# Optimization experiments

Measured on AMD Instinct MI355X. Metric: run time of the kernel, lower is better.

Reference implementation:

```python
import jax, jax.numpy as jnp
import numpy as np

D_MODEL = 1024
N_HEADS = 16
WINDOW = 256
SSM_N = 256
EPS = 1e-5


def _layernorm(x, g, b):
    m = x.mean(-1, keepdims=True)
    v = ((x - m) ** 2).mean(-1, keepdims=True)
    return (x - m) / jnp.sqrt(v + EPS) * g + b


def _sliding_window_attn(Q, K, V, W):
    # Q,K,V: [B,h,T,dh]; exact sliding-window causal attention (keys q-W+1..q)
    B, h, T, dh = Q.shape
    nb = T // W
    Qb = Q.reshape(B, h, nb, W, dh)
    pad = jnp.zeros((B, h, W, dh), Q.dtype)
    Kp = jnp.concatenate([pad, K], axis=2)  # [B,h,T+W,dh]
    Kprev = Kp[:, :, :T].reshape(B, h, nb, W, dh)
    Kcur = K.reshape(B, h, nb, W, dh)
    Kwin = jnp.concatenate([Kprev, Kcur], axis=3)  # [B,h,nb,2W,dh]
    Vp = jnp.concatenate([pad, V], axis=2)
    Vprev = Vp[:, :, :T].reshape(B, h, nb, W, dh)
    Vcur = V.reshape(B, h, nb, W, dh)
    Vwin = jnp.concatenate([Vprev, Vcur], axis=3)
    scores = jnp.einsum('bhnid,bhnjd->bhnij', Qb, Kwin) / jnp.sqrt(jnp.asarray(dh, Q.dtype))
    i = jnp.arange(W)[:, None]
    j = jnp.arange(2 * W)[None, :]
    blk = jnp.arange(nb)[:, None, None]
    # key global pos = blk*W - W + j ; valid iff i < j <= i+W and key pos >= 0
    mask = (j > i) & (j <= i + W) & (blk * W - W + j >= 0)  # [nb,W,2W]
    neg = jnp.asarray(jnp.finfo(scores.dtype).min, scores.dtype)
    scores = jnp.where(mask[None, None], scores, neg)
    p = jax.nn.softmax(scores, axis=-1)
    out = jnp.einsum('bhnij,bhnjd->bhnid', p, Vwin)
    return out.reshape(B, h, T, dh)


def _forward(x, ssm_state, ln1_g, ln1_b, ln2_g, ln2_b, wq, bq, wk, bk, wv, bv,
             wo, bo, wg, bg, A, Bw, Cw, w1, b1, w2, b2):
    B, T, d = x.shape
    h = N_HEADS
    dh = d // h
    xn = _layernorm(x, ln1_g, ln1_b)
    # windowed attention path
    Q = (xn @ wq + bq).reshape(B, T, h, dh).transpose(0, 2, 1, 3)
    K = (xn @ wk + bk).reshape(B, T, h, dh).transpose(0, 2, 1, 3)
    V = (xn @ wv + bv).reshape(B, T, h, dh).transpose(0, 2, 1, 3)
    ao = _sliding_window_attn(Q, K, V, WINDOW)
    y_attn = ao.transpose(0, 2, 1, 3).reshape(B, T, d) @ wo + bo
    # SSM path: s_t = tanh(A)*s_{t-1} + B x_t ; y_t = C s_t
    alpha = jnp.tanh(A)
    u = xn @ Bw  # [B,T,N]
    def step(s, u_t):
        s = alpha * s + u_t
        return s, s
    new_state, states = jax.lax.scan(step, ssm_state, u.transpose(1, 0, 2))
    y_ssm = states.transpose(1, 0, 2) @ Cw  # [B,T,d]
    # gated fusion + residual
    g = jax.nn.sigmoid(xn @ wg + bg)
    y = g * y_attn + (1.0 - g) * y_ssm
    x = x + y
    # Pre-LN MLP
    x2 = _layernorm(x, ln2_g, ln2_b)
    x = x + jax.nn.gelu(x2 @ w1 + b1, approximate=False) @ w2 + b2
    return x, new_state


def setup_inputs() -> dict:
    key = jax.random.key(0)
    ks = jax.random.split(key, 16)
    B, T, d, N = 2, 2048, D_MODEL, SSM_N
    s = 0.02
    inp = {
        'x': jax.random.normal(ks[0], (B, T, d), jnp.float32),
        'ssm_state': jnp.zeros((B, N), jnp.float32),
        'ln1_g': jnp.ones((d,), jnp.float32),
        'ln1_b': jnp.zeros((d,), jnp.float32),
        'ln2_g': jnp.ones((d,), jnp.float32),
        'ln2_b': jnp.zeros((d,), jnp.float32),
        'wq': jax.random.normal(ks[1], (d, d), jnp.float32) * s,
        'bq': jnp.zeros((d,), jnp.float32),
        'wk': jax.random.normal(ks[2], (d, d), jnp.float32) * s,
        'bk': jnp.zeros((d,), jnp.float32),
        'wv': jax.random.normal(ks[3], (d, d), jnp.float32) * s,
        'bv': jnp.zeros((d,), jnp.float32),
        'wo': jax.random.normal(ks[4], (d, d), jnp.float32) * s,
        'bo': jnp.zeros((d,), jnp.float32),
        'wg': jax.random.normal(ks[5], (d, d), jnp.float32) * s,
        'bg': jnp.zeros((d,), jnp.float32),
        'A': jax.random.uniform(ks[6], (N,), jnp.float32, -0.1, 0.1),
        'Bw': jax.random.normal(ks[7], (d, N), jnp.float32) * s,
        'Cw': jax.random.normal(ks[8], (N, d), jnp.float32) * s,
        'w1': jax.random.normal(ks[9], (d, 4 * d), jnp.float32) * s,
        'b1': jnp.zeros((4 * d,), jnp.float32),
        'w2': jax.random.normal(ks[10], (4 * d, d), jnp.float32) * s,
        'b2': jnp.zeros((d,), jnp.float32),
    }
    return inp


def reference(x, ssm_state, ln1_g, ln1_b, ln2_g, ln2_b, wq, bq, wk, bk, wv, bv,
              wo, bo, wg, bg, A, Bw, Cw, w1, b1, w2, b2):
    return _forward(x, ssm_state, ln1_g, ln1_b, ln2_g, ln2_b, wq, bq, wk, bk,
                    wv, bv, wo, bo, wg, bg, A, Bw, Cw, w1, b1, w2, b2)
```

## Files before the change

kernel.cpp:

```cpp
#include <hip/hip_runtime.h>
#include <math.h>

#define BB 2
#define TT 2048
#define DD 1024
#define HH 16
#define DH 64
#define WW 256
#define NN 256
#define ROWS (BB*TT)
#define ROWSZ ((size_t)ROWS*DD)
#define NQU 4352

typedef unsigned short u16;
typedef __attribute__((ext_vector_type(8))) short short8;
typedef __attribute__((ext_vector_type(4))) float f32x4;

__device__ __forceinline__ float bf2f(u16 h) {
    union { unsigned int u; float f; } c; c.u = ((unsigned int)h) << 16; return c.f;
}
__device__ __forceinline__ u16 f2bf(float f) {
    union { float f; unsigned int u; } c; c.f = f;
    unsigned int r = c.u + 0x7fffu + ((c.u >> 16) & 1u);
    return (u16)(r >> 16);
}

__device__ __forceinline__ void gld16(const void* g, void* l) {
    __builtin_amdgcn_global_load_lds(
        (const __attribute__((address_space(1))) void*)g,
        (__attribute__((address_space(3))) void*)l, 16, 0, 0);
}

#define WAITB(N) asm volatile("s_waitcnt vmcnt(" #N ")\n\ts_barrier" ::: "memory")

__global__ __launch_bounds__(256) void ln_kernel(const float* __restrict__ x,
                                                 const float* __restrict__ g,
                                                 const float* __restrict__ b,
                                                 u16* __restrict__ out) {
    int row = blockIdx.x;
    int t = threadIdx.x;
    const float4* xr = (const float4*)(x + (size_t)row * DD);
    float4 v4 = xr[t];
    float s  = v4.x + v4.y + v4.z + v4.w;
    float s2 = v4.x*v4.x + v4.y*v4.y + v4.z*v4.z + v4.w*v4.w;
    #pragma unroll
    for (int o = 32; o > 0; o >>= 1) { s += __shfl_xor(s, o); s2 += __shfl_xor(s2, o); }
    __shared__ float red[2][4];
    int wid = t >> 6, lane = t & 63;
    if (lane == 0) { red[0][wid] = s; red[1][wid] = s2; }
    __syncthreads();
    s  = red[0][0] + red[0][1] + red[0][2] + red[0][3];
    s2 = red[1][0] + red[1][1] + red[1][2] + red[1][3];
    float mean = s * (1.0f / DD);
    float var  = s2 * (1.0f / DD) - mean * mean;
    float inv  = rsqrtf(var + 1e-5f);
    const float4* g4 = (const float4*)g;
    const float4* b4 = (const float4*)b;
    float4 gg = g4[t], bb = b4[t];
    float o0 = (v4.x - mean) * inv * gg.x + bb.x;
    float o1 = (v4.y - mean) * inv * gg.y + bb.y;
    float o2 = (v4.z - mean) * inv * gg.z + bb.z;
    float o3 = (v4.w - mean) * inv * gg.w + bb.w;
    uint2 packed;
    packed.x = (unsigned)f2bf(o0) | ((unsigned)f2bf(o1) << 16);
    packed.y = (unsigned)f2bf(o2) | ((unsigned)f2bf(o3) << 16);
    *(uint2*)(out + (size_t)row * DD + 4 * t) = packed;
}

__global__ __launch_bounds__(256) void tconv_all(
    const float* __restrict__ wq, const float* __restrict__ wk,
    const float* __restrict__ wv, const float* __restrict__ wg,
    const float* __restrict__ Bw, const float* __restrict__ wo,
    const float* __restrict__ Cw, const float* __restrict__ w1,
    const float* __restrict__ w2,
    u16* __restrict__ wqkvgut, u16* __restrict__ wot, u16* __restrict__ cwt,
    u16* __restrict__ w1t, u16* __restrict__ w2t) {
    int tile = blockIdx.x;
    const float* src; u16* dst; int K, N, tx, ty;
    if (tile < 4096) {
        int seg = tile >> 10, tl = tile & 1023;
        src = (seg == 0) ? wq : (seg == 1) ? wk : (seg == 2) ? wv : wg;
        dst = wqkvgut + (size_t)seg * 1024 * 1024;
        K = 1024; N = 1024; tx = tl & 31; ty = tl >> 5;
    } else if (tile < 4352) {
        int tl = tile - 4096;
        src = Bw; dst = wqkvgut + (size_t)4096 * 1024;
        K = 1024; N = 256; tx = tl & 7; ty = tl >> 3;
    } else if (tile < 5376) {
        int tl = tile - 4352;
        src = wo; dst = wot; K = 1024; N = 1024; tx = tl & 31; ty = tl >> 5;
    } else if (tile < 5632) {
        int tl = tile - 5376;
        src = Cw; dst = cwt; K = 256; N = 1024; tx = tl & 31; ty = tl >> 5;
    } else if (tile < 9728) {
        int tl = tile - 5632;
        src = w1; dst = w1t; K = 1024; N = 4096; tx = tl & 127; ty = tl >> 7;
    } else {
        int tl = tile - 9728;
        src = w2; dst = w2t; K = 4096; N = 1024; tx = tl & 31; ty = tl >> 5;
    }
    __shared__ float ts[32][33];
    int n0 = tx * 32, k0 = ty * 32;
    int tc = threadIdx.x & 31, tr = threadIdx.x >> 5;
    #pragma unroll
    for (int i = tr; i < 32; i += 8)
        ts[i][tc] = src[(size_t)(k0 + i) * N + n0 + tc];
    __syncthreads();
    #pragma unroll
    for (int i = tr; i < 32; i += 8)
        dst[(size_t)(n0 + i) * K + k0 + tc] = f2bf(ts[tc][i]);
}

__global__ __launch_bounds__(256) void bias_init(const float* __restrict__ bq,
                                                 const float* __restrict__ bk,
                                                 const float* __restrict__ bv,
                                                 const float* __restrict__ bg,
                                                 float* __restrict__ dst) {
    int i = blockIdx.x * 256 + threadIdx.x;
    if (i >= NQU) return;
    float v = 0.f;
    if (i < 1024) v = bq[i];
    else if (i < 2048) v = bk[i - 1024];
    else if (i < 3072) v = bv[i - 2048];
    else if (i < 4096) v = bg[i - 3072];
    dst[i] = v;
}

__device__ __forceinline__ void gemm_core_pipe(const u16* __restrict__ A,
                                               const u16* __restrict__ Bt,
                                               int K, int kiters, int kofs,
                                               int m0, int n0,
                                               short (*Als)[128][32],
                                               short (*Bls)[128][32],
                                               int t, f32x4 acc[4][4]) {
    int lane = t & 63, w = t >> 6;
    int wr = w >> 1, wc = w & 1;
    int jq = lane >> 4, rq = lane & 15;
    int swzb = (jq ^ ((rq >> 1) & 3)) << 4;
    const char* gA[2]; const char* gB[2];
    int lofs[2];
    #pragma unroll
    for (int i = 0; i < 2; i++) {
        int s = i * 256 + t;
        int r = s >> 2, p = s & 3;
        int j = p ^ ((r >> 1) & 3);
        gA[i] = (const char*)(A + (size_t)(m0 + r) * K + kofs) + j * 16;
        gB[i] = (const char*)(Bt + (size_t)(n0 + r) * K + kofs) + j * 16;
        lofs[i] = s * 16;
    }
    #pragma unroll
    for (int i = 0; i < 2; i++) {
        gld16(gA[i], (char*)(Als + 0) + lofs[i]);
        gld16(gB[i], (char*)(Bls + 0) + lofs[i]);
    }
    if (kiters > 1) {
        #pragma unroll
        for (int i = 0; i < 2; i++) {
            gld16(gA[i] + 64, (char*)(Als + 1) + lofs[i]);
            gld16(gB[i] + 64, (char*)(Bls + 1) + lofs[i]);
        }
    }
    for (int kt = 0; kt < kiters; kt++) {
        if (kt + 1 < kiters) { WAITB(4); } else { WAITB(0); }
        if (kt + 2 < kiters) {
            int q = (kt + 2) % 3;
            size_t ko = (size_t)(kt + 2) * 64;
            #pragma unroll
            for (int i = 0; i < 2; i++) {
                gld16(gA[i] + ko, (char*)(Als + q) + lofs[i]);
                gld16(gB[i] + ko, (char*)(Bls + q) + lofs[i]);
            }
        }
        int p = kt % 3;
        const char* Ab = (const char*)(Als + p);
        const char* Bb = (const char*)(Bls + p);
        short8 af[4], bfr[4];
        #pragma unroll
        for (int i = 0; i < 4; i++) {
            af[i]  = *(const short8*)(Ab + (wr * 64 + i * 16 + rq) * 64 + swzb);
            bfr[i] = *(const short8*)(Bb + (wc * 64 + i * 16 + rq) * 64 + swzb);
        }
        #pragma unroll
        for (int i = 0; i < 4; i++)
            #pragma unroll
            for (int jn = 0; jn < 4; jn++)
                acc[i][jn] = __builtin_amdgcn_mfma_f32_16x16x32_bf16(af[i], bfr[jn], acc[i][jn], 0, 0, 0);
    }
}

template<int ACT, bool OUTBF, bool SPLIT>
__global__ __launch_bounds__(256) void mgemm64(const u16* __restrict__ A,
                                               const u16* __restrict__ Bt,
                                               const float* __restrict__ bias,
                                               void* __restrict__ C,
                                               int M, int N, int K, int Kslice,
                                               int mtiles, int ntiles, int PM, int PN) {
    __shared__ __align__(16) short Als[3][128][32];
    __shared__ __align__(16) short Bls[3][128][32];
    int t = threadIdx.x;
    int l = blockIdx.x;
    int xcd = l & 7, li = l >> 3;
    int rm = mtiles / PM, rn = ntiles / PN;
    int xm = xcd % PM, xn = xcd / PM;
    int mt = xm * rm + li % rm;
    int nt = xn * rn + li / rm;
    int m0 = mt * 128, n0 = nt * 128;
    int z = SPLIT ? blockIdx.y : 0;
    f32x4 acc[4][4];
    #pragma unroll
    for (int i = 0; i < 4; i++)
        #pragma unroll
        for (int j = 0; j < 4; j++)
            acc[i][j] = (f32x4){0.f, 0.f, 0.f, 0.f};
    gemm_core_pipe(A, Bt, K, Kslice >> 5, z * Kslice, m0, n0, Als, Bls, t, acc);

    int lane = t & 63, w = t >> 6;
    int wr = w >> 1, wc = w & 1;
    int jq = lane >> 4, rq = lane & 15;
    u16* Cb = OUTBF ? ((u16*)C + (SPLIT ? (size_t)z * M * N : (size_t)0)) : nullptr;
    float* Cf = (float*)C;
    #pragma unroll
    for (int i = 0; i < 4; i++) {
        int rowb = m0 + wr * 64 + i * 16 + jq * 4;
        #pragma unroll
        for (int jn = 0; jn < 4; jn++) {
            int col = n0 + wc * 64 + jn * 16 + rq;
            float bv = bias ? bias[col] : 0.f;
            #pragma unroll
            for (int rr = 0; rr < 4; rr++) {
                float v = acc[i][jn][rr] + bv;
                if (ACT == 1) v = 0.5f * v * (1.0f + erff(v * 0.70710678118654752f));
                size_t off = (size_t)(rowb + rr) * N + col;
                if (OUTBF) Cb[off] = f2bf(v);
                else Cf[off] = v;
            }
        }
    }
}

__global__ __launch_bounds__(256) void proj3(const u16* __restrict__ ao,
                                             const u16* __restrict__ states,
                                             const u16* __restrict__ wot,
                                             const u16* __restrict__ cwt,
                                             const float* __restrict__ bo,
                                             u16* __restrict__ ya0,
                                             u16* __restrict__ ya1,
                                             float* __restrict__ ys) {
    __shared__ __align__(16) short Als[3][128][32];
    __shared__ __align__(16) short Bls[3][128][32];
    int t = threadIdx.x;
    int m0 = blockIdx.y * 128, n0 = blockIdx.x * 128;
    int z = blockIdx.z;
    const u16* A; const u16* Bt; int K, kofs, kiters;
    if (z < 2) { A = ao; Bt = wot; K = 1024; kofs = z * 512; kiters = 16; }
    else       { A = states; Bt = cwt; K = 256; kofs = 0; kiters = 8; }
    f32x4 acc[4][4];
    #pragma unroll
    for (int i = 0; i < 4; i++)
        #pragma unroll
        for (int j = 0; j < 4; j++)
            acc[i][j] = (f32x4){0.f, 0.f, 0.f, 0.f};
    gemm_core_pipe(A, Bt, K, kiters, kofs, m0, n0, Als, Bls, t, acc);

    int lane = t & 63, w = t >> 6;
    int wr = w >> 1, wc = w & 1;
    int jq = lane >> 4, rq = lane & 15;
    u16* dst = (z == 0) ? ya0 : ya1;
    #pragma unroll
    for (int i = 0; i < 4; i++) {
        int rowb = m0 + wr * 64 + i * 16 + jq * 4;
        #pragma unroll
        for (int jn = 0; jn < 4; jn++) {
            int col = n0 + wc * 64 + jn * 16 + rq;
            float bv = (z == 0) ? bo[col] : 0.f;
            #pragma unroll
            for (int rr = 0; rr < 4; rr++) {
                float v = acc[i][jn][rr] + bv;
                size_t off = (size_t)(rowb + rr) * DD + col;
                if (z < 2) dst[off] = f2bf(v);
                else ys[off] = v;
            }
        }
    }
}

__global__ __launch_bounds__(256) void attn_scan(const u16* __restrict__ QKVG,
                                                 u16* __restrict__ O,
                                                 const float* __restrict__ Assm,
                                                 const float* __restrict__ s0,
                                                 u16* __restrict__ states,
                                                 float* __restrict__ s_out) {
    __shared__ __align__(16) short Qs[8][64][8];
    __shared__ __align__(16) short Ks[8][64][8];
    __shared__ __align__(16) short Vt[64][72];
    __shared__ __align__(16) short Ps[4][16][72];

    if (blockIdx.x >= 1024) {
        int idx = (blockIdx.x - 1024) * 256 + threadIdx.x;
        int n = idx & 255;
        int c = (idx >> 8) & 31;
        int b = idx >> 13;
        float alpha = tanhf(Assm[n]);
        int t0 = c * 64;
        float s = (c == 0) ? s0[b * NN + n] : 0.f;
        const u16* up = QKVG + (size_t)(b * TT) * NQU + 4096 + n;
        if (c > 0) {
            #pragma unroll
            for (int k = 8; k >= 1; k--)
                s = alpha * s + bf2f(up[(size_t)(t0 - k) * NQU]);
        }
        u16* sp = states + (size_t)(b * TT) * NN + n;
        for (int t = t0; t < t0 + 64; t++) {
            s = alpha * s + bf2f(up[(size_t)t * NQU]);
            sp[(size_t)t * NN] = f2bf(s);
        }
        if (c == 31) s_out[b * NN + n] = s;
        return;
    }

    int blk = blockIdx.x;
    int qb = blk & 31;
    int h  = (blk >> 5) & 15;
    int b  = blk >> 9;
    int q0 = qb * 64;
    int t = threadIdx.x, lane = t & 63, w = t >> 6;
    int rq = lane & 15, jq = lane >> 4;

    const size_t RS = NQU;

    #pragma unroll
    for (int i = 0; i < 2; i++) {
        int c = 2 * w + i;
        const u16* g = QKVG + (size_t)(b * TT + q0 + lane) * RS + h * 64 + c * 8;
        gld16(g, (char*)Qs + c * 1024);
    }

    f32x4 Oa[4];
    #pragma unroll
    for (int tj = 0; tj < 4; tj++) Oa[tj] = (f32x4){0.f, 0.f, 0.f, 0.f};
    float mrow[4], lrow[4];
    #pragma unroll
    for (int r = 0; r < 4; r++) { mrow[r] = -1e30f; lrow[r] = 0.f; }

    int c0 = 4 - (q0 >> 6); if (c0 < 0) c0 = 0;

    for (int ci = c0; ci < 5; ci++) {
        int kbase = q0 - 256 + ci * 64;
        #pragma unroll
        for (int i = 0; i < 2; i++) {
            int c = 2 * w + i;
            const u16* g = QKVG + (size_t)(b * TT + kbase + lane) * RS + 1024 + h * 64 + c * 8;
            gld16(g, (char*)Ks + c * 1024);
        }
        #pragma unroll
        for (int i = 0; i < 2; i++) {
            int dhg = i * 4 + w;
            uint4 v = *(const uint4*)(QKVG + (size_t)(b * TT + kbase + lane) * RS + 2048 + h * 64 + dhg * 8);
            const u16* pv = (const u16*)&v;
            #pragma unroll
            for (int j = 0; j < 8; j++) Vt[dhg * 8 + j][lane] = (short)pv[j];
        }
        __syncthreads();

        short8 qf[2];
        #pragma unroll
        for (int s = 0; s < 2; s++)
            qf[s] = *(const short8*)&Qs[4 * s + jq][w * 16 + rq][0];

        f32x4 S[4];
        #pragma unroll
        for (int tj = 0; tj < 4; tj++) S[tj] = (f32x4){0.f, 0.f, 0.f, 0.f};
        #pragma unroll
        for (int s = 0; s < 2; s++)
            #pragma unroll
            for (int tj = 0; tj < 4; tj++) {
                short8 kf = *(const short8*)&Ks[4 * s + jq][tj * 16 + rq][0];
                S[tj] = __builtin_amdgcn_mfma_f32_16x16x32_bf16(qf[s], kf, S[tj], 0, 0, 0);
            }

        #pragma unroll
        for (int r = 0; r < 4; r++) {
            int q = q0 + w * 16 + jq * 4 + r;
            float sv[4];
            #pragma unroll
            for (int tj = 0; tj < 4; tj++) {
                int kp = kbase + tj * 16 + rq;
                float x = S[tj][r] * 0.125f;
                bool valid = (kp <= q) && (kp > q - WW);
                sv[tj] = valid ? x : -1e30f;
            }
            float cm = fmaxf(fmaxf(sv[0], sv[1]), fmaxf(sv[2], sv[3]));
            #pragma unroll
            for (int o = 1; o < 16; o <<= 1) cm = fmaxf(cm, __shfl_xor(cm, o));
            float mn = fmaxf(mrow[r], cm);
            bool any = mn > -1e29f;
            float al = any ? __expf(mrow[r] - mn) : 1.f;
            float ps = 0.f;
            #pragma unroll
            for (int tj = 0; tj < 4; tj++) {
                float p = any ? __expf(sv[tj] - mn) : 0.f;
                ps += p;
                Ps[w][jq * 4 + r][tj * 16 + rq] = (short)f2bf(p);
            }
            #pragma unroll
            for (int o = 1; o < 16; o <<= 1) ps += __shfl_xor(ps, o);
            lrow[r] = lrow[r] * al + ps;
            mrow[r] = mn;
            #pragma unroll
            for (int tj = 0; tj < 4; tj++) Oa[tj][r] *= al;
        }

        #pragma unroll
        for (int s = 0; s < 2; s++) {
            short8 pf = *(const short8*)&Ps[w][rq][32 * s + 8 * jq];
            #pragma unroll
            for (int tj = 0; tj < 4; tj++) {
                short8 vf = *(const short8*)&Vt[tj * 16 + rq][32 * s + 8 * jq];
                Oa[tj] = __builtin_amdgcn_mfma_f32_16x16x32_bf16(pf, vf, Oa[tj], 0, 0, 0);
            }
        }
        __syncthreads();
    }

    #pragma unroll
    for (int r = 0; r < 4; r++) {
        int q = q0 + w * 16 + jq * 4 + r;
        float inv = 1.f / lrow[r];
        #pragma unroll
        for (int tj = 0; tj < 4; tj++)
            O[(size_t)(b * TT + q) * DD + h * 64 + tj * 16 + rq] = f2bf(Oa[tj][r] * inv);
    }
}

__global__ __launch_bounds__(256) void fuse_ln2(const float* __restrict__ x,
                                                const u16* __restrict__ QKVG,
                                                const u16* __restrict__ ya0,
                                                const u16* __restrict__ ya1,
                                                const float* __restrict__ ys,
                                                const float* __restrict__ g2,
                                                const float* __restrict__ b2,
                                                float* __restrict__ out,
                                                u16* __restrict__ x2n) {
    int row = blockIdx.x, t = threadIdx.x;
    float4 xv = ((const float4*)(x + (size_t)row * DD))[t];
    uint2 gw = *(const uint2*)(QKVG + (size_t)row * NQU + 3072 + 4 * t);
    uint2 a0 = *(const uint2*)(ya0 + (size_t)row * DD + 4 * t);
    uint2 a1 = *(const uint2*)(ya1 + (size_t)row * DD + 4 * t);
    float4 sv = ((const float4*)(ys + (size_t)row * DD))[t];
    u16 gh[4] = {(u16)(gw.x & 0xffff), (u16)(gw.x >> 16), (u16)(gw.y & 0xffff), (u16)(gw.y >> 16)};
    u16 ah[4] = {(u16)(a0.x & 0xffff), (u16)(a0.x >> 16), (u16)(a0.y & 0xffff), (u16)(a0.y >> 16)};
    u16 bh[4] = {(u16)(a1.x & 0xffff), (u16)(a1.x >> 16), (u16)(a1.y & 0xffff), (u16)(a1.y >> 16)};
    float xe[4] = {xv.x, xv.y, xv.z, xv.w};
    float se[4] = {sv.x, sv.y, sv.z, sv.w};
    float o[4];
    #pragma unroll
    for (int e = 0; e < 4; e++) {
        float g = 1.0f / (1.0f + __expf(-bf2f(gh[e])));
        float a = bf2f(ah[e]) + bf2f(bh[e]);
        o[e] = xe[e] + g * a + (1.0f - g) * se[e];
    }
    float s = o[0] + o[1] + o[2] + o[3];
    float s2 = o[0]*o[0] + o[1]*o[1] + o[2]*o[2] + o[3]*o[3];
    #pragma unroll
    for (int off = 32; off > 0; off >>= 1) { s += __shfl_xor(s, off); s2 += __shfl_xor(s2, off); }
    __shared__ float red[2][4];
    int wid = t >> 6, lane = t & 63;
    if (lane == 0) { red[0][wid] = s; red[1][wid] = s2; }
    __syncthreads();
    s  = red[0][0] + red[0][1] + red[0][2] + red[0][3];
    s2 = red[1][0] + red[1][1] + red[1][2] + red[1][3];
    float mean = s * (1.0f / DD);
    float var  = s2 * (1.0f / DD) - mean * mean;
    float inv  = rsqrtf(var + 1e-5f);
    float4 gg = ((const float4*)g2)[t];
    float4 bb = ((const float4*)b2)[t];
    float ge[4] = {gg.x, gg.y, gg.z, gg.w};
    float be[4] = {bb.x, bb.y, bb.z, bb.w};
    float4 ov = {o[0], o[1], o[2], o[3]};
    ((float4*)(out + (size_t)row * DD))[t] = ov;
    u16 nh[4];
    #pragma unroll
    for (int e = 0; e < 4; e++) nh[e] = f2bf((o[e] - mean) * inv * ge[e] + be[e]);
    uint2 packed;
    packed.x = (unsigned)nh[0] | ((unsigned)nh[1] << 16);
    packed.y = (unsigned)nh[2] | ((unsigned)nh[3] << 16);
    *(uint2*)(x2n + (size_t)row * DD + 4 * t) = packed;
}

__global__ __launch_bounds__(256) void mlp2_reduce(const u16* __restrict__ pbase,
                                                   const float* __restrict__ b2,
                                                   float* __restrict__ out) {
    size_t i4 = (size_t)blockIdx.x * 256 + threadIdx.x;
    float4 o = ((float4*)out)[i4];
    float4 bb = ((const float4*)b2)[i4 & 255];
    float acc0 = bb.x, acc1 = bb.y, acc2 = bb.z, acc3 = bb.w;
    #pragma unroll
    for (int z = 0; z < 4; z++) {
        uint2 p = ((const uint2*)(pbase + (size_t)z * ROWSZ))[i4];
        acc0 += bf2f((u16)(p.x & 0xffff));
        acc1 += bf2f((u16)(p.x >> 16));
        acc2 += bf2f((u16)(p.y & 0xffff));
        acc3 += bf2f((u16)(p.y >> 16));
    }
    o.x += acc0; o.y += acc1; o.z += acc2; o.w += acc3;
    ((float4*)out)[i4] = o;
}

extern "C" void kernel_launch(void* const* d_in, const int* in_sizes, int n_in,
                              void* d_out, int out_size, void* d_ws, size_t ws_size,
                              hipStream_t stream) {
    const float* x     = (const float*)d_in[0];
    const float* sst   = (const float*)d_in[1];
    const float* ln1g  = (const float*)d_in[2];
    const float* ln1b  = (const float*)d_in[3];
    const float* ln2g  = (const float*)d_in[4];
    const float* ln2b  = (const float*)d_in[5];
    const float* wq    = (const float*)d_in[6];
    const float* bq    = (const float*)d_in[7];
    const float* wk    = (const float*)d_in[8];
    const float* bk    = (const float*)d_in[9];
    const float* wv    = (const float*)d_in[10];
    const float* bv    = (const float*)d_in[11];
    const float* wo    = (const float*)d_in[12];
    const float* bo    = (const float*)d_in[13];
    const float* wg    = (const float*)d_in[14];
    const float* bg    = (const float*)d_in[15];
    const float* A     = (const float*)d_in[16];
    const float* Bw    = (const float*)d_in[17];
    const float* Cw    = (const float*)d_in[18];
    const float* w1    = (const float*)d_in[19];
    const float* b1    = (const float*)d_in[20];
    const float* w2    = (const float*)d_in[21];
    const float* b2    = (const float*)d_in[22];

    float* out = (float*)d_out;
    char* ws = (char*)d_ws;
    const size_t KBs = 1024;

    u16*   QKVGU  = (u16*)(ws);
    u16*   ya0b   = (u16*)(ws + 34816 * KBs);
    u16*   ya1b   = (u16*)(ws + 43008 * KBs);
    float* ys     = (float*)(ws + 51200 * KBs);
    u16*   parts  = ya0b;
    u16*   xn     = (u16*)(ws + 67584 * KBs);
    u16*   ao     = (u16*)(ws + 75776 * KBs);
    u16*   states = (u16*)(ws + 83968 * KBs);
    u16*   wqkvgut= (u16*)(ws + 86016 * KBs);
    u16*   wot    = (u16*)(ws + 94720 * KBs);
    u16*   cwt    = (u16*)(ws + 96768 * KBs);
    u16*   w1t    = (u16*)(ws + 97280 * KBs);
    u16*   w2t    = (u16*)(ws + 105472 * KBs);
    float* biasq  = (float*)(ws + 113664 * KBs);
    u16*   x2n    = xn;
    u16*   h1     = QKVGU;

    float* new_state_out = out + ROWSZ;

    hipLaunchKernelGGL(tconv_all, dim3(13824), dim3(256), 0, stream,
                       wq, wk, wv, wg, Bw, wo, Cw, w1, w2,
                       wqkvgut, wot, cwt, w1t, w2t);
    hipLaunchKernelGGL(bias_init, dim3(17), dim3(256), 0, stream, bq, bk, bv, bg, biasq);

    hipLaunchKernelGGL(ln_kernel, dim3(ROWS), dim3(256), 0, stream, x, ln1g, ln1b, xn);
    hipLaunchKernelGGL((mgemm64<0,true,false>), dim3(1088, 1), dim3(256), 0, stream,
                       xn, wqkvgut, biasq, (void*)QKVGU, ROWS, NQU, 1024, 1024,
                       32, 34, 4, 2);
    hipLaunchKernelGGL(attn_scan, dim3(1088), dim3(256), 0, stream,
                       QKVGU, ao, A, sst, states, new_state_out);
    hipLaunchKernelGGL(proj3, dim3(8, 32, 3), dim3(256), 0, stream,
                       ao, states, wot, cwt, bo, ya0b, ya1b, ys);
    hipLaunchKernelGGL(fuse_ln2, dim3(ROWS), dim3(256), 0, stream,
                       x, QKVGU, ya0b, ya1b, ys, ln2g, ln2b, out, x2n);
    hipLaunchKernelGGL((mgemm64<1,true,false>), dim3(1024, 1), dim3(256), 0, stream,
                       x2n, w1t, b1, (void*)h1, ROWS, 4*DD, 1024, 1024,
                       32, 32, 4, 2);
    hipLaunchKernelGGL((mgemm64<0,true,true>), dim3(256, 4), dim3(256), 0, stream,
                       h1, w2t, (const float*)nullptr, (void*)parts, ROWS, DD, 4096, 1024,
                       32, 8, 8, 1);
    hipLaunchKernelGGL(mlp2_reduce, dim3(4096), dim3(256), 0, stream, parts, b2, out);
}
```

Before: 422.7 us.

## Use single-buffer occupancy-oriented GEMM core and split SSM input projection out

The triple-buffered, waitcnt-pipelined GEMM core is replaced by a single-stage LDS buffer (16 KB instead of 48 KB). It uses two __syncthreads per k-step and issues the next tile's loads before the MFMAs. Launch bounds now request 4 blocks per CU, trading explicit prefetch depth for more resident waves to hide latency. Separately, the 256-column SSM input projection is removed from the fused QKVG GEMM, so row stride drops from 4352 to 4096. That projection now runs as its own split-K GEMM followed by a bf16 reduce kernel, adding a launch and extra rounding of the partial sums.

```diff
diff --git a/kernel.cpp b/kernel.cpp
--- a/kernel.cpp
+++ b/kernel.cpp
@@ -10,7 +10,6 @@
 #define NN 256
 #define ROWS (BB*TT)
 #define ROWSZ ((size_t)ROWS*DD)
-#define NQU 4352
 
 typedef unsigned short u16;
 typedef __attribute__((ext_vector_type(8))) short short8;
@@ -30,8 +29,6 @@
         (const __attribute__((address_space(1))) void*)g,
         (__attribute__((address_space(3))) void*)l, 16, 0, 0);
 }
-
-#define WAITB(N) asm volatile("s_waitcnt vmcnt(" #N ")\n\ts_barrier" ::: "memory")
 
 __global__ __launch_bounds__(256) void ln_kernel(const float* __restrict__ x,
                                                  const float* __restrict__ g,
@@ -117,86 +114,80 @@
                                                  const float* __restrict__ bg,
                                                  float* __restrict__ dst) {
     int i = blockIdx.x * 256 + threadIdx.x;
-    if (i >= NQU) return;
-    float v = 0.f;
+    if (i >= 4096) return;
+    float v;
     if (i < 1024) v = bq[i];
     else if (i < 2048) v = bk[i - 1024];
     else if (i < 3072) v = bv[i - 2048];
-    else if (i < 4096) v = bg[i - 3072];
+    else v = bg[i - 3072];
     dst[i] = v;
 }
 
-__device__ __forceinline__ void gemm_core_pipe(const u16* __restrict__ A,
-                                               const u16* __restrict__ Bt,
-                                               int K, int kiters, int kofs,
-                                               int m0, int n0,
-                                               short (*Als)[128][32],
-                                               short (*Bls)[128][32],
-                                               int t, f32x4 acc[4][4]) {
+__device__ __forceinline__ void gemm_core_97(const u16* __restrict__ A,
+                                             const u16* __restrict__ Bt,
+                                             int K, int kiters, int kofs,
+                                             int m0, int n0,
+                                             char* Als, char* Bls,
+                                             int t, f32x4 acc[4][4]) {
     int lane = t & 63, w = t >> 6;
     int wr = w >> 1, wc = w & 1;
     int jq = lane >> 4, rq = lane & 15;
-    int swzb = (jq ^ ((rq >> 1) & 3)) << 4;
-    const char* gA[2]; const char* gB[2];
-    int lofs[2];
-    #pragma unroll
-    for (int i = 0; i < 2; i++) {
-        int s = i * 256 + t;
+    int csw = (jq ^ ((rq >> 1) & 3)) << 4;
+    int rowA[4], rowB[4];
+    #pragma unroll
+    for (int i = 0; i < 4; i++) {
+        rowA[i] = (wr * 64 + i * 16 + rq) * 64;
+        rowB[i] = (wc * 64 + i * 16 + rq) * 64;
+    }
+    const char* gA[2]; const char* gB[2]; int lof[2];
+    #pragma unroll
+    for (int c = 0; c < 2; c++) {
+        int s = c * 256 + t;
         int r = s >> 2, p = s & 3;
         int j = p ^ ((r >> 1) & 3);
-        gA[i] = (const char*)(A + (size_t)(m0 + r) * K + kofs) + j * 16;
-        gB[i] = (const char*)(Bt + (size_t)(n0 + r) * K + kofs) + j * 16;
-        lofs[i] = s * 16;
-    }
-    #pragma unroll
-    for (int i = 0; i < 2; i++) {
-        gld16(gA[i], (char*)(Als + 0) + lofs[i]);
-        gld16(gB[i], (char*)(Bls + 0) + lofs[i]);
-    }
-    if (kiters > 1) {
-        #pragma unroll
-        for (int i = 0; i < 2; i++) {
-            gld16(gA[i] + 64, (char*)(Als + 1) + lofs[i]);
-            gld16(gB[i] + 64, (char*)(Bls + 1) + lofs[i]);
-        }
+        gA[c] = (const char*)(A + (size_t)(m0 + r) * K + kofs) + j * 16;
+        gB[c] = (const char*)(Bt + (size_t)(n0 + r) * K + kofs) + j * 16;
+        lof[c] = s * 16;
+    }
+    #pragma unroll
+    for (int c = 0; c < 2; c++) {
+        gld16(gA[c], Als + lof[c]);
+        gld16(gB[c], Bls + lof[c]);
     }
     for (int kt = 0; kt < kiters; kt++) {
-        if (kt + 1 < kiters) { WAITB(4); } else { WAITB(0); }
-        if (kt + 2 < kiters) {
-            int q = (kt + 2) % 3;
-            size_t ko = (size_t)(kt + 2) * 64;
-            #pragma unroll
-            for (int i = 0; i < 2; i++) {
-                gld16(gA[i] + ko, (char*)(Als + q) + lofs[i]);
-                gld16(gB[i] + ko, (char*)(Bls + q) + lofs[i]);
-            }
-        }
-        int p = kt % 3;
-        const char* Ab = (const char*)(Als + p);
-        const char* Bb = (const char*)(Bls + p);
-        short8 af[4], bfr[4];
+        __syncthreads();
+        short8 af[4], bf[4];
         #pragma unroll
         for (int i = 0; i < 4; i++) {
-            af[i]  = *(const short8*)(Ab + (wr * 64 + i * 16 + rq) * 64 + swzb);
-            bfr[i] = *(const short8*)(Bb + (wc * 64 + i * 16 + rq) * 64 + swzb);
+            af[i] = *(const short8*)(Als + rowA[i] + csw);
+            bf[i] = *(const short8*)(Bls + rowB[i] + csw);
+        }
+        __syncthreads();
+        if (kt + 1 < kiters) {
+            size_t ko = (size_t)(kt + 1) * 64;
+            #pragma unroll
+            for (int c = 0; c < 2; c++) {
+                gld16(gA[c] + ko, Als + lof[c]);
+                gld16(gB[c] + ko, Bls + lof[c]);
+            }
         }
         #pragma unroll
         for (int i = 0; i < 4; i++)
             #pragma unroll
-            for (int jn = 0; jn < 4; jn++)
-                acc[i][jn] = __builtin_amdgcn_mfma_f32_16x16x32_bf16(af[i], bfr[jn], acc[i][jn], 0, 0, 0);
+            for (int j = 0; j < 4; j++)
+                acc[i][j] = __builtin_amdgcn_mfma_f32_16x16x32_bf16(af[i], bf[j], acc[i][j], 0, 0, 0);
     }
 }
 
 template<int ACT, bool OUTBF, bool SPLIT>
-__global__ __launch_bounds__(256) void mgemm64(const u16* __restrict__ A,
-                                               const u16* __restrict__ Bt,
-                                               const float* __restrict__ bias,
-                                               void* __restrict__ C,
-                                               int M, int N, int K, int Kslice,
-                                               int mtiles, int ntiles, int PM, int PN) {
-    __shared__ __align__(16) short Als[3][128][32];
-    __shared__ __align__(16) short Bls[3][128][32];
+__global__ __launch_bounds__(256, 4) void mgemm64(const u16* __restrict__ A,
+                                                  const u16* __restrict__ Bt,
+                                                  const float* __restrict__ bias,
+                                                  void* __restrict__ C,
+                                                  int M, int N, int K, int Kslice,
+                                                  int mtiles, int ntiles, int PM, int PN) {
+    __shared__ __align__(16) char Als[8192];
+    __shared__ __align__(16) char Bls[8192];
     int t = threadIdx.x;
     int l = blockIdx.x;
     int xcd = l & 7, li = l >> 3;
@@ -212,7 +203,7 @@
         #pragma unroll
         for (int j = 0; j < 4; j++)
             acc[i][j] = (f32x4){0.f, 0.f, 0.f, 0.f};
-    gemm_core_pipe(A, Bt, K, Kslice >> 5, z * Kslice, m0, n0, Als, Bls, t, acc);
+    gemm_core_97(A, Bt, K, Kslice >> 5, z * Kslice, m0, n0, Als, Bls, t, acc);
 
     int lane = t & 63, w = t >> 6;
     int wr = w >> 1, wc = w & 1;
@@ -238,16 +229,34 @@
     }
 }
 
-__global__ __launch_bounds__(256) void proj3(const u16* __restrict__ ao,
-                                             const u16* __restrict__ states,
-                                             const u16* __restrict__ wot,
-                                             const u16* __restrict__ cwt,
-                                             const float* __restrict__ bo,
-                                             u16* __restrict__ ya0,
-                                             u16* __restrict__ ya1,
-                                             float* __restrict__ ys) {
-    __shared__ __align__(16) short Als[3][128][32];
-    __shared__ __align__(16) short Bls[3][128][32];
+__global__ __launch_bounds__(256) void ureduce(const u16* __restrict__ p,
+                                               u16* __restrict__ o) {
+    size_t i2 = (size_t)blockIdx.x * 256 + threadIdx.x;
+    float a0 = 0.f, a1 = 0.f, a2 = 0.f, a3 = 0.f;
+    #pragma unroll
+    for (int z = 0; z < 4; z++) {
+        uint2 v = ((const uint2*)(p + (size_t)z * 1048576))[i2];
+        a0 += bf2f((u16)(v.x & 0xffff));
+        a1 += bf2f((u16)(v.x >> 16));
+        a2 += bf2f((u16)(v.y & 0xffff));
+        a3 += bf2f((u16)(v.y >> 16));
+    }
+    uint2 r;
+    r.x = (unsigned)f2bf(a0) | ((unsigned)f2bf(a1) << 16);
+    r.y = (unsigned)f2bf(a2) | ((unsigned)f2bf(a3) << 16);
+    ((uint2*)o)[i2] = r;
+}
+
+__global__ __launch_bounds__(256, 4) void proj3(const u16* __restrict__ ao,
+                                                const u16* __restrict__ states,
+                                                const u16* __restrict__ wot,
+                                                const u16* __restrict__ cwt,
+                                                const float* __restrict__ bo,
+                                                u16* __restrict__ ya0,
+                                                u16* __restrict__ ya1,
+                                                float* __restrict__ ys) {
+    __shared__ __align__(16) char Als[8192];
+    __shared__ __align__(16) char Bls[8192];
     int t = threadIdx.x;
     int m0 = blockIdx.y * 128, n0 = blockIdx.x * 128;
     int z = blockIdx.z;
@@ -260,7 +269,7 @@
         #pragma unroll
         for (int j = 0; j < 4; j++)
             acc[i][j] = (f32x4){0.f, 0.f, 0.f, 0.f};
-    gemm_core_pipe(A, Bt, K, kiters, kofs, m0, n0, Als, Bls, t, acc);
+    gemm_core_97(A, Bt, K, kiters, kofs, m0, n0, Als, Bls, t, acc);
 
     int lane = t & 63, w = t >> 6;
     int wr = w >> 1, wc = w & 1;
@@ -285,6 +294,7 @@
 }
 
 __global__ __launch_bounds__(256) void attn_scan(const u16* __restrict__ QKVG,
+                                                 const u16* __restrict__ ubuf,
                                                  u16* __restrict__ O,
                                                  const float* __restrict__ Assm,
                                                  const float* __restrict__ s0,
@@ -303,15 +313,15 @@
         float alpha = tanhf(Assm[n]);
         int t0 = c * 64;
         float s = (c == 0) ? s0[b * NN + n] : 0.f;
-        const u16* up = QKVG + (size_t)(b * TT) * NQU + 4096 + n;
+        const u16* up = ubuf + (size_t)(b * TT) * NN + n;
         if (c > 0) {
             #pragma unroll
             for (int k = 8; k >= 1; k--)
-                s = alpha * s + bf2f(up[(size_t)(t0 - k) * NQU]);
+                s = alpha * s + bf2f(up[(size_t)(t0 - k) * NN]);
         }
         u16* sp = states + (size_t)(b * TT) * NN + n;
         for (int t = t0; t < t0 + 64; t++) {
-            s = alpha * s + bf2f(up[(size_t)t * NQU]);
+            s = alpha * s + bf2f(up[(size_t)t * NN]);
             sp[(size_t)t * NN] = f2bf(s);
         }
         if (c == 31) s_out[b * NN + n] = s;
@@ -326,7 +336,7 @@
     int t = threadIdx.x, lane = t & 63, w = t >> 6;
     int rq = lane & 15, jq = lane >> 4;
 
-    const size_t RS = NQU;
+    const size_t RS = 4096;
 
     #pragma unroll
     for (int i = 0; i < 2; i++) {
@@ -443,7 +453,7 @@
                                                 u16* __restrict__ x2n) {
     int row = blockIdx.x, t = threadIdx.x;
     float4 xv = ((const float4*)(x + (size_t)row * DD))[t];
-    uint2 gw = *(const uint2*)(QKVG + (size_t)row * NQU + 3072 + 4 * t);
+    uint2 gw = *(const uint2*)(QKVG + (size_t)row * 4096 + 3072 + 4 * t);
     uint2 a0 = *(const uint2*)(ya0 + (size_t)row * DD + 4 * t);
     uint2 a1 = *(const uint2*)(ya1 + (size_t)row * DD + 4 * t);
     float4 sv = ((const float4*)(ys + (size_t)row * DD))[t];
@@ -537,10 +547,11 @@
     char* ws = (char*)d_ws;
     const size_t KBs = 1024;
 
-    u16*   QKVGU  = (u16*)(ws);
+    u16*   QKVG   = (u16*)(ws);
     u16*   ya0b   = (u16*)(ws + 34816 * KBs);
     u16*   ya1b   = (u16*)(ws + 43008 * KBs);
     float* ys     = (float*)(ws + 51200 * KBs);
+    u16*   uparts = ya0b;
     u16*   parts  = ya0b;
     u16*   xn     = (u16*)(ws + 67584 * KBs);
     u16*   ao     = (u16*)(ws + 75776 * KBs);
@@ -552,25 +563,31 @@
     u16*   w2t    = (u16*)(ws + 105472 * KBs);
     float* biasq  = (float*)(ws + 113664 * KBs);
     u16*   x2n    = xn;
-    u16*   h1     = QKVGU;
+    u16*   ubuf   = xn;
+    u16*   h1     = QKVG;
 
     float* new_state_out = out + ROWSZ;
 
     hipLaunchKernelGGL(tconv_all, dim3(13824), dim3(256), 0, stream,
                        wq, wk, wv, wg, Bw, wo, Cw, w1, w2,
                        wqkvgut, wot, cwt, w1t, w2t);
-    hipLaunchKernelGGL(bias_init, dim3(17), dim3(256), 0, stream, bq, bk, bv, bg, biasq);
+    hipLaunchKernelGGL(bias_init, dim3(16), dim3(256), 0, stream, bq, bk, bv, bg, biasq);
 
     hipLaunchKernelGGL(ln_kernel, dim3(ROWS), dim3(256), 0, stream, x, ln1g, ln1b, xn);
-    hipLaunchKernelGGL((mgemm64<0,true,false>), dim3(1088, 1), dim3(256), 0, stream,
-                       xn, wqkvgut, biasq, (void*)QKVGU, ROWS, NQU, 1024, 1024,
-                       32, 34, 4, 2);
+    hipLaunchKernelGGL((mgemm64<0,true,false>), dim3(1024, 1), dim3(256), 0, stream,
+                       xn, wqkvgut, biasq, (void*)QKVG, ROWS, 4096, 1024, 1024,
+                       32, 32, 4, 2);
+    hipLaunchKernelGGL((mgemm64<0,true,true>), dim3(64, 4), dim3(256), 0, stream,
+                       xn, wqkvgut + (size_t)4096 * 1024, (const float*)nullptr,
+                       (void*)uparts, ROWS, 256, 1024, 256,
+                       32, 2, 8, 1);
+    hipLaunchKernelGGL(ureduce, dim3(1024), dim3(256), 0, stream, uparts, ubuf);
     hipLaunchKernelGGL(attn_scan, dim3(1088), dim3(256), 0, stream,
-                       QKVGU, ao, A, sst, states, new_state_out);
+                       QKVG, ubuf, ao, A, sst, states, new_state_out);
     hipLaunchKernelGGL(proj3, dim3(8, 32, 3), dim3(256), 0, stream,
                        ao, states, wot, cwt, bo, ya0b, ya1b, ys);
     hipLaunchKernelGGL(fuse_ln2, dim3(ROWS), dim3(256), 0, stream,
-                       x, QKVGU, ya0b, ya1b, ys, ln2g, ln2b, out, x2n);
+                       x, QKVG, ya0b, ya1b, ys, ln2g, ln2b, out, x2n);
     hipLaunchKernelGGL((mgemm64<1,true,false>), dim3(1024, 1), dim3(256), 0, stream,
                        x2n, w1t, b1, (void*)h1, ROWS, 4*DD, 1024, 1024,
                        32, 32, 4, 2);
```

Result: faster. 395.5 us (-6.5%).
